# Kernel optimization log

Measured on AMD Instinct MI355X. Metric: run time of the kernel, lower is better.

## Reference

```python
import jax, jax.numpy as jnp
import numpy as np
from jax import lax

K = 8          # num_classes
C_IN = 256     # in_channels
EPS = 1e-5


def resize_bilinear_ac(x, H, W):
    """Bilinear resize with align_corners=True. x: [B,C,h,w] -> [B,C,H,W]."""
    B, C, h, w = x.shape
    if h == H and w == W:
        return x
    ys = jnp.linspace(0.0, h - 1.0, H)
    xs = jnp.linspace(0.0, w - 1.0, W)
    y0 = jnp.floor(ys).astype(jnp.int32)
    x0 = jnp.floor(xs).astype(jnp.int32)
    y1 = jnp.minimum(y0 + 1, h - 1)
    x1 = jnp.minimum(x0 + 1, w - 1)
    wy = (ys - y0.astype(x.dtype))[None, None, :, None]
    wx = (xs - x0.astype(x.dtype))[None, None, None, :]
    g00 = x[:, :, y0][:, :, :, x0]
    g01 = x[:, :, y0][:, :, :, x1]
    g10 = x[:, :, y1][:, :, :, x0]
    g11 = x[:, :, y1][:, :, :, x1]
    top = g00 * (1.0 - wx) + g01 * wx
    bot = g10 * (1.0 - wx) + g11 * wx
    return top * (1.0 - wy) + bot * wy


def setup_inputs() -> dict:
    key = jax.random.key(0)
    ks = jax.random.split(key, 16)
    shapes = [(2, 256, 128, 128), (2, 256, 64, 64), (2, 256, 32, 32), (2, 256, 16, 16), (2, 256, 8, 8)]
    inp = {}
    for i, s in enumerate(shapes):
        inp[f"feat{i}"] = jax.random.normal(ks[i], s, dtype=jnp.float32)
    inp["attr_feat"] = jax.random.normal(ks[5], (2, K * C_IN, 64, 64), dtype=jnp.float32)
    # learned params
    inp["mlp_f_w"] = jax.random.normal(ks[6], (256, 256), dtype=jnp.float32) * 0.02
    inp["mlp_f_b"] = jnp.zeros((256,), dtype=jnp.float32)
    inp["mlp_a_w"] = jax.random.normal(ks[7], (256, 256), dtype=jnp.float32) * 0.02
    inp["mlp_a_b"] = jnp.zeros((256,), dtype=jnp.float32)
    # 5 grouped convs: [out=2048, in_per_group=256, 3, 3] each, no bias (BN follows)
    inp["conv_w"] = jax.random.normal(ks[8], (5, K * C_IN, C_IN, 3, 3), dtype=jnp.float32) * 0.02
    inp["bn_gamma"] = jnp.ones((5, K * C_IN), dtype=jnp.float32)
    inp["bn_beta"] = jnp.zeros((5, K * C_IN), dtype=jnp.float32)
    inp["bn_mean"] = jax.random.normal(ks[9], (5, K * C_IN), dtype=jnp.float32) * 0.1
    inp["bn_var"] = jax.random.uniform(ks[10], (5, K * C_IN), dtype=jnp.float32, minval=0.5, maxval=1.5)
    return inp


def _forward(feats, attr_feat, mlp_f_w, mlp_f_b, mlp_a_w, mlp_a_b, conv_w, bn_gamma, bn_beta, bn_mean, bn_var):
    B = attr_feat.shape[0]
    # global avg pool attr -> [B, K, C] -> mlp_a
    avg_attr = attr_feat.mean(axis=(2, 3)).reshape(B, K, C_IN)
    avg_attr = avg_attr @ mlp_a_w.T + mlp_a_b  # [B,K,256]
    outs = []
    for i, x in enumerate(feats):
        _, C, H, W = x.shape
        avg_x = x.mean(axis=(2, 3)) @ mlp_f_w.T + mlp_f_b          # [B,256]
        logits = jnp.einsum('bkc,bc->bk', avg_attr, avg_x)          # [B,K]
        attn = jax.nn.softmax(logits, axis=-1)
        y = resize_bilinear_ac(attr_feat, H, W)                      # [B,2048,H,W]
        y = lax.conv_general_dilated(
            y, conv_w[i], window_strides=(1, 1), padding=((1, 1), (1, 1)),
            dimension_numbers=('NCHW', 'OIHW', 'NCHW'), feature_group_count=K)
        inv = lax.rsqrt(bn_var[i] + EPS)
        y = (y - bn_mean[i][None, :, None, None]) * (inv * bn_gamma[i])[None, :, None, None] + bn_beta[i][None, :, None, None]
        y = jax.nn.relu(y)
        y = y.reshape(B, K, C, H, W)
        y = jnp.einsum('bkchw,bk->bchw', y, attn)                   # weighted sum over classes
        outs.append(jax.nn.relu(x + y))
    return tuple(outs)


def reference(feat0, feat1, feat2, feat3, feat4, attr_feat, mlp_f_w, mlp_f_b, mlp_a_w, mlp_a_b, conv_w, bn_gamma, bn_beta, bn_mean, bn_var):
    feats = [feat0, feat1, feat2, feat3, feat4]
    return _forward(feats, attr_feat, mlp_f_w, mlp_f_b, mlp_a_w, mlp_a_b, conv_w, bn_gamma, bn_beta, bn_mean, bn_var)
```

## Files before the change

### kernel.cpp

```cpp
#include <hip/hip_runtime.h>
#include <hip/hip_bf16.h>
#include <cstdint>

typedef __attribute__((ext_vector_type(8))) short short8;
typedef __attribute__((ext_vector_type(4))) float f32x4;

#define EPSV 1e-5f

__device__ __forceinline__ void gload_lds16(const void* g, void* l) {
  __builtin_amdgcn_global_load_lds(
      (const __attribute__((address_space(1))) void*)(uintptr_t)g,
      (__attribute__((address_space(3))) void*)(uint32_t)(uintptr_t)l,
      16, 0, 0);
}

__device__ __forceinline__ uint32_t f2bf_rne(float v) {
  const uint32_t u = __float_as_uint(v);
  const uint32_t r = ((u >> 16) & 1u) + 0x7fffu;
  return (u + r) >> 16;
}

__global__ void mean_kernel(const float* __restrict__ in, float* __restrict__ out,
                            int HW, float inv) {
  const int ch = blockIdx.x;
  const int t = threadIdx.x;
  const float* p = in + (size_t)ch * HW;
  float s = 0.f;
  const int nv = HW >> 2;
  const float4* pv = (const float4*)p;
  for (int i = t; i < nv; i += 256) { float4 v = pv[i]; s += v.x + v.y + v.z + v.w; }
  __shared__ float red[256];
  red[t] = s; __syncthreads();
  for (int off = 128; off > 0; off >>= 1) {
    if (t < off) red[t] += red[t + off];
    __syncthreads();
  }
  if (t == 0) out[ch] = red[0] * inv;
}

__global__ void wtrans_kernel(const float* __restrict__ cw,
                              const float* __restrict__ gamma, const float* __restrict__ beta,
                              const float* __restrict__ mean, const float* __restrict__ var,
                              __hip_bfloat16* __restrict__ wt, float* __restrict__ bias) {
  const int oc = blockIdx.x;
  const int i  = blockIdx.y;
  const int ci = threadIdx.x;
  const int idx = i * 2048 + oc;
  const float sc = rsqrtf(var[idx] + EPSV) * gamma[idx];
  if (ci == 0) bias[idx] = beta[idx] - mean[idx] * sc;
  const int g = oc >> 8, co = oc & 255;
  const float* src = cw + ((size_t)idx * 256 + ci) * 9;
  const size_t dbase = (size_t)(i * 8 + g) * 9 * 65536 + co * 256 + ci;
#pragma unroll
  for (int tap = 0; tap < 9; ++tap)
    wt[dbase + (size_t)tap * 65536] = __float2bfloat16(src[tap] * sc);
}

__global__ void gate_kernel(const float* __restrict__ meanA, const float* __restrict__ meanF,
                            const float* __restrict__ Wa, const float* __restrict__ ba,
                            const float* __restrict__ Wf, const float* __restrict__ bfp,
                            float* __restrict__ attn) {
  __shared__ float mA[16 * 256];
  __shared__ float mF[10 * 256];
  __shared__ float pA[16 * 256];
  __shared__ float pF[10 * 256];
  __shared__ float lg[80];
  const int t = threadIdx.x;
  for (int i = t; i < 4096; i += 256) mA[i] = meanA[i];
  for (int i = t; i < 2560; i += 256) mF[i] = meanF[i];
  __syncthreads();
  {
    float acc[16];
#pragma unroll
    for (int j = 0; j < 16; ++j) acc[j] = 0.f;
    for (int ci = 0; ci < 256; ++ci) {
      const float w = Wa[t * 256 + ci];
#pragma unroll
      for (int j = 0; j < 16; ++j) acc[j] += mA[j * 256 + ci] * w;
    }
    const float bb = ba[t];
#pragma unroll
    for (int j = 0; j < 16; ++j) pA[j * 256 + t] = acc[j] + bb;
  }
  {
    float acc[10];
#pragma unroll
    for (int j = 0; j < 10; ++j) acc[j] = 0.f;
    for (int ci = 0; ci < 256; ++ci) {
      const float w = Wf[t * 256 + ci];
#pragma unroll
      for (int j = 0; j < 10; ++j) acc[j] += mF[j * 256 + ci] * w;
    }
    const float bb = bfp[t];
#pragma unroll
    for (int j = 0; j < 10; ++j) pF[j * 256 + t] = acc[j] + bb;
  }
  __syncthreads();
  if (t < 80) {
    const int i = t >> 4, r = t & 15, b = r >> 3, k = r & 7;
    const float* a = &pA[(b * 8 + k) * 256];
    const float* f = &pF[(i * 2 + b) * 256];
    float d = 0.f;
    for (int c = 0; c < 256; ++c) d += a[c] * f[c];
    lg[t] = d;
  }
  __syncthreads();
  if (t < 10) {
    const int base = t * 8;
    float m = lg[base];
    for (int k = 1; k < 8; ++k) m = fmaxf(m, lg[base + k]);
    float e[8], s = 0.f;
    for (int k = 0; k < 8; ++k) { e[k] = __expf(lg[base + k] - m); s += e[k]; }
    const float invs = 1.f / s;
    for (int k = 0; k < 8; ++k) attn[base + k] = e[k] * invs;
  }
}

__global__ void resize_kernel(const float* __restrict__ attr,
                              __hip_bfloat16* __restrict__ R,
                              int W, int Hp, int Wp, float scl) {
  const int bk = blockIdx.x;
  const int yp = blockIdx.y;
  const int t  = threadIdx.x;
  const size_t rowbase = ((size_t)bk * Hp + yp) * (size_t)Wp * 256;
  if (yp == 0 || yp == Hp - 1) {
    uint32_t* p = (uint32_t*)(R + rowbase);
    const int n = Wp * 128;
    for (int idx = t; idx < n; idx += 256) p[idx] = 0u;
    return;
  }
  const int y = yp - 1;
  const float fy = y * scl;
  int y0 = (int)floorf(fy); if (y0 > 63) y0 = 63;
  const float wy = fy - (float)y0;
  const int y1 = min(y0 + 1, 63);
  __shared__ float buf[2][64][65];
  const int cc = t >> 2, seg = (t & 3) * 16;
  const int bb = bk >> 3, k = bk & 7;
  const float* ab = attr + (size_t)bb * 2048 * 4096;
  const int ci = t & 63;
  for (int cq = 0; cq < 4; ++cq) {
    __syncthreads();
    {
      const int ch = k * 256 + cq * 64 + cc;
      const float* r0 = ab + ((size_t)ch * 64 + y0) * 64;
      const float* r1 = ab + ((size_t)ch * 64 + y1) * 64;
#pragma unroll
      for (int u = 0; u < 4; ++u) {
        float4 v0 = ((const float4*)r0)[(t & 3) * 4 + u];
        float4 v1 = ((const float4*)r1)[(t & 3) * 4 + u];
        buf[0][cc][seg + u * 4 + 0] = v0.x; buf[0][cc][seg + u * 4 + 1] = v0.y;
        buf[0][cc][seg + u * 4 + 2] = v0.z; buf[0][cc][seg + u * 4 + 3] = v0.w;
        buf[1][cc][seg + u * 4 + 0] = v1.x; buf[1][cc][seg + u * 4 + 1] = v1.y;
        buf[1][cc][seg + u * 4 + 2] = v1.z; buf[1][cc][seg + u * 4 + 3] = v1.w;
      }
    }
    __syncthreads();
    for (int x = t >> 6; x < W; x += 4) {
      const float fx = x * scl;
      int x0 = (int)floorf(fx); if (x0 > 63) x0 = 63;
      const float wx = fx - (float)x0;
      const int x1 = min(x0 + 1, 63);
      const float top = buf[0][ci][x0] * (1.f - wx) + buf[0][ci][x1] * wx;
      const float bot = buf[1][ci][x0] * (1.f - wx) + buf[1][ci][x1] * wx;
      R[rowbase + (size_t)(x + 1) * 256 + cq * 64 + ci] = __float2bfloat16(top * (1.f - wy) + bot * wy);
    }
    if (t < 64) {
      R[rowbase + cq * 64 + t] = __float2bfloat16(0.f);
      R[rowbase + (size_t)(Wp - 1) * 256 + cq * 64 + t] = __float2bfloat16(0.f);
    }
  }
}

__device__ __forceinline__ void coords36(int u, int g0, int& g, int& ty, int& tx, int& cq) {
  g = g0 + u / 36;
  const int r = u % 36;
  const int tap = r >> 2;
  cq = r & 3;
  ty = tap / 3;
  tx = tap - ty * 3;
}

__global__ __launch_bounds__(512, 1)
void conv256_kernel(const __hip_bfloat16* __restrict__ R,
                    const __hip_bfloat16* __restrict__ Wt,
                    const float* __restrict__ bias,
                    const float* __restrict__ attn,
                    __hip_bfloat16* __restrict__ zout,
                    int W, int lw, int Hp, int Wp, int HW,
                    int NB, int gcount) {
  __shared__ alignas(16) __hip_bfloat16 ldsA[2][256 * 64];
  __shared__ alignas(16) __hip_bfloat16 ldsB[2][256 * 64];
  const int tid  = threadIdx.x;
  const int lane = tid & 63;
  const int wave = __builtin_amdgcn_readfirstlane(tid >> 6);
  const int wm = (wave >> 2) * 128;
  const int wn = (wave & 3) * 64;

  const int nx  = gridDim.x;
  const int lin = blockIdx.x;
  const int pos = ((nx & 7) == 0) ? ((lin & 7) * (nx >> 3) + (lin >> 3)) : lin;
  const int n0  = pos * 256;

  const int bb = (int)blockIdx.y % NB;
  const int gs = (int)blockIdx.y / NB;
  const int g0 = gs * gcount;

  const int c8 = lane & 7, r8 = lane >> 3;
  const int sc = (c8 ^ r8) << 3;
  const int aoff0 = ((wave * 32 + r8) << 8) + sc;
  const int dst0  = wave * 2048;
  int boff[4];
#pragma unroll
  for (int q = 0; q < 4; ++q) {
    const int row = wave * 32 + q * 8 + r8;
    const int sg = n0 + row;
    const int y = sg >> lw, x = sg & (W - 1);
    boff[q] = ((y * Wp + x) << 8) + sc;
  }

  const size_t rgstride = (size_t)Hp * Wp * 256;
  const __hip_bfloat16* Rb = R + (size_t)bb * 8 * rgstride;

  const f32x4 fz = {0.f, 0.f, 0.f, 0.f};
  f32x4 acc[8][4];
  uint32_t finp[8][4][2];
#pragma unroll
  for (int mf = 0; mf < 8; ++mf)
#pragma unroll
    for (int nf = 0; nf < 4; ++nf) {
      acc[mf][nf] = fz; finp[mf][nf][0] = 0u; finp[mf][nf][1] = 0u;
    }

  const int nk = gcount * 36;
  {
    const __hip_bfloat16* wp = Wt + ((size_t)g0 * 9 << 16);
    const __hip_bfloat16* rp = Rb + (size_t)g0 * rgstride;
#pragma unroll
    for (int q = 0; q < 4; ++q) gload_lds16(wp + aoff0 + q * 2048, &ldsA[0][dst0 + q * 512]);
#pragma unroll
    for (int q = 0; q < 4; ++q) gload_lds16(rp + boff[q], &ldsB[0][dst0 + q * 512]);
  }

  int foldc = 0, gcur = g0;
  for (int t = 0; t < nk; ++t) {
    const int c = t & 1;
    const bool pf = (t + 1 < nk);
    int g1, ty1, tx1, cq1;
    coords36(pf ? t + 1 : t, g0, g1, ty1, tx1, cq1);
    const __hip_bfloat16* wp1 = Wt + (((size_t)g1 * 9 + ty1 * 3 + tx1) << 16) + (cq1 << 6);
    const __hip_bfloat16* rp1 = Rb + (size_t)g1 * rgstride + ((ty1 * Wp + tx1) << 8) + (cq1 << 6);

    asm volatile("s_waitcnt vmcnt(0)" ::: "memory");
    __builtin_amdgcn_s_barrier();
    asm volatile("" ::: "memory");

    const __hip_bfloat16* pA = &ldsA[c][0];
    const __hip_bfloat16* pB = &ldsB[c][0];
    __hip_bfloat16* dA = &ldsA[c ^ 1][0];
    __hip_bfloat16* dB = &ldsB[c ^ 1][0];

#pragma unroll
    for (int ks = 0; ks < 2; ++ks) {
      const int cb = ks * 4 + (lane >> 4);
      short8 bfv[4];
#pragma unroll
      for (int nf = 0; nf < 4; ++nf) {
        const int row = wn + nf * 16 + (lane & 15);
        bfv[nf] = *(const short8*)&pB[(row << 6) + ((cb ^ (row & 7)) << 3)];
      }
#pragma unroll
      for (int h = 0; h < 2; ++h) {
        short8 af[4];
#pragma unroll
        for (int m = 0; m < 4; ++m) {
          const int row = wm + (h * 4 + m) * 16 + (lane & 15);
          af[m] = *(const short8*)&pA[(row << 6) + ((cb ^ (row & 7)) << 3)];
        }
        if (ks == 0 && pf) {
          if (h == 0) {
#pragma unroll
            for (int q = 0; q < 4; ++q) gload_lds16(wp1 + aoff0 + q * 2048, dA + dst0 + q * 512);
          } else {
#pragma unroll
            for (int q = 0; q < 4; ++q) gload_lds16(rp1 + boff[q], dB + dst0 + q * 512);
          }
        }
        __builtin_amdgcn_s_barrier();
        __builtin_amdgcn_sched_barrier(0);
        __builtin_amdgcn_s_setprio(1);
#pragma unroll
        for (int m = 0; m < 4; ++m)
#pragma unroll
          for (int nf = 0; nf < 4; ++nf)
            acc[h * 4 + m][nf] = __builtin_amdgcn_mfma_f32_16x16x32_bf16(
                af[m], bfv[nf], acc[h * 4 + m][nf], 0, 0, 0);
        __builtin_amdgcn_s_setprio(0);
        __builtin_amdgcn_s_barrier();
        asm volatile("" ::: "memory");
      }
    }

    if (++foldc == 36) {
      foldc = 0;
      const float aw = attn[bb * 8 + gcur];
#pragma unroll
      for (int mf = 0; mf < 8; ++mf) {
        const int cobase = wm + mf * 16 + ((lane >> 4) << 2);
#pragma unroll
        for (int pr = 0; pr < 2; ++pr) {
          const float b0v = bias[(gcur << 8) + cobase + pr * 2 + 0];
          const float b1v = bias[(gcur << 8) + cobase + pr * 2 + 1];
#pragma unroll
          for (int nf = 0; nf < 4; ++nf) {
            const uint32_t p = finp[mf][nf][pr];
            const float f0 = __uint_as_float(p << 16)
                           + aw * fmaxf(acc[mf][nf][pr * 2 + 0] + b0v, 0.f);
            const float f1 = __uint_as_float(p & 0xffff0000u)
                           + aw * fmaxf(acc[mf][nf][pr * 2 + 1] + b1v, 0.f);
            finp[mf][nf][pr] = (f2bf_rne(f1) << 16) | f2bf_rne(f0);
          }
        }
#pragma unroll
        for (int nf = 0; nf < 4; ++nf) acc[mf][nf] = fz;
      }
      ++gcur;
    }
  }

  __hip_bfloat16* zb = zout + (size_t)(gs * 2 + bb) * 256 * (size_t)HW;
#pragma unroll
  for (int mf = 0; mf < 8; ++mf) {
    const int cobase = wm + mf * 16 + ((lane >> 4) << 2);
#pragma unroll
    for (int nf = 0; nf < 4; ++nf) {
      const int n = n0 + wn + nf * 16 + (lane & 15);
#pragma unroll
      for (int pr = 0; pr < 2; ++pr) {
        const uint32_t p = finp[mf][nf][pr];
        zb[(size_t)(cobase + pr * 2 + 0) * HW + n] =
            __float2bfloat16(__uint_as_float(p << 16));
        zb[(size_t)(cobase + pr * 2 + 1) * HW + n] =
            __float2bfloat16(__uint_as_float(p & 0xffff0000u));
      }
    }
  }
}

__global__ __launch_bounds__(256, 2)
void conv_kernel(const __hip_bfloat16* __restrict__ R,
                 const __hip_bfloat16* __restrict__ Wt,
                 const float* __restrict__ bias,
                 const float* __restrict__ attn,
                 const float* __restrict__ featp,
                 void* __restrict__ outp,
                 int W, int lw, int Hp, int Wp, int HW,
                 int b0, int NB, int gcount) {
  __shared__ alignas(16) __hip_bfloat16 ldsA[2][128 * 64];
  __shared__ alignas(16) __hip_bfloat16 ldsB[3][128 * 64];
  const int tid  = threadIdx.x;
  const int lane = tid & 63;
  const int wave = __builtin_amdgcn_readfirstlane(tid >> 6);
  const int wm = (wave >> 1) * 64;
  const int wn = (wave & 1) * 64;

  const int nx  = gridDim.x;
  const int lin = blockIdx.x;
  const int pos = ((nx & 7) == 0) ? ((lin & 7) * (nx >> 3) + (lin >> 3)) : lin;
  const int co0 = (pos & 1) * 128;
  const int n0  = (pos >> 1) * 128;

  const int bb  = (int)blockIdx.y % NB;
  const int gs  = (int)blockIdx.y / NB;
  const int b   = b0 + bb;
  const int g0  = gs * gcount;

  const int c8 = lane & 7;
  const int r8 = lane >> 3;
  int aoff[4], boff[4], dst[4];
#pragma unroll
  for (int q = 0; q < 4; ++q) {
    const int row = (wave * 4 + q) * 8 + r8;
    const int sc = (c8 ^ (row & 7)) << 3;
    aoff[q] = ((co0 + row) << 8) + sc;
    int sg = n0 + row; if (sg >= HW) sg = HW - 1;
    const int y = sg >> lw, x = sg & (W - 1);
    boff[q] = ((y * Wp + x) << 8) + sc;
    dst[q] = (wave * 4 + q) * 512;
  }

  const size_t rgstride = (size_t)Hp * Wp * 256;
  const __hip_bfloat16* Rb = R + (size_t)bb * 8 * rgstride;

  const f32x4 fz = {0.f, 0.f, 0.f, 0.f};
  f32x4 fin[4][4], acc[4][4];
#pragma unroll
  for (int mf = 0; mf < 4; ++mf)
#pragma unroll
    for (int nf = 0; nf < 4; ++nf) { fin[mf][nf] = fz; acc[mf][nf] = fz; }

  const int nstages = gcount * 36;
  {
    int g, ty, tx, cq;
    coords36(0, g0, g, ty, tx, cq);
    const __hip_bfloat16* wp = Wt + (((size_t)g * 9 + ty * 3 + tx) << 16) + (cq << 6);
    const __hip_bfloat16* rp = Rb + (size_t)g * rgstride + ((ty * Wp + tx) << 8) + (cq << 6);
#pragma unroll
    for (int q = 0; q < 4; ++q) gload_lds16(wp + aoff[q], &ldsA[0][dst[q]]);
#pragma unroll
    for (int q = 0; q < 4; ++q) gload_lds16(rp + boff[q], &ldsB[0][dst[q]]);
    coords36(1 < nstages ? 1 : 0, g0, g, ty, tx, cq);
    const __hip_bfloat16* rp1 = Rb + (size_t)g * rgstride + ((ty * Wp + tx) << 8) + (cq << 6);
#pragma unroll
    for (int q = 0; q < 4; ++q) gload_lds16(rp1 + boff[q], &ldsB[1][dst[q]]);
  }

  int bcur = 0, b2 = 2;
  int foldc = 0, gcur = g0;

  for (int s = 0; s < nstages; ++s) {
    __builtin_amdgcn_s_barrier();
    asm volatile("" ::: "memory");
    if (s + 1 < nstages) {
      int g, ty, tx, cq;
      coords36(s + 1, g0, g, ty, tx, cq);
      const __hip_bfloat16* wp = Wt + (((size_t)g * 9 + ty * 3 + tx) << 16) + (cq << 6);
      __hip_bfloat16* dA = &ldsA[(s + 1) & 1][0];
#pragma unroll
      for (int q = 0; q < 4; ++q) gload_lds16(wp + aoff[q], dA + dst[q]);
    }
    if (s + 2 < nstages) {
      int g, ty, tx, cq;
      coords36(s + 2, g0, g, ty, tx, cq);
      const __hip_bfloat16* rp = Rb + (size_t)g * rgstride + ((ty * Wp + tx) << 8) + (cq << 6);
      __hip_bfloat16* dB = &ldsB[b2][0];
#pragma unroll
      for (int q = 0; q < 4; ++q) gload_lds16(rp + boff[q], dB + dst[q]);
    }
    if (s + 2 < nstages)      asm volatile("s_waitcnt vmcnt(12)" ::: "memory");
    else if (s + 1 < nstages) asm volatile("s_waitcnt vmcnt(8)" ::: "memory");
    else                      asm volatile("s_waitcnt vmcnt(0)" ::: "memory");
    __builtin_amdgcn_s_barrier();
    asm volatile("" ::: "memory");

    const __hip_bfloat16* pA = &ldsA[s & 1][0];
    const __hip_bfloat16* pB = &ldsB[bcur][0];
#pragma unroll
    for (int ks = 0; ks < 2; ++ks) {
      short8 af[4], bfv[4];
      const int cb = ks * 4 + (lane >> 4);
#pragma unroll
      for (int mf = 0; mf < 4; ++mf) {
        const int row = wm + mf * 16 + (lane & 15);
        af[mf] = *(const short8*)&pA[(row << 6) + ((cb ^ (row & 7)) << 3)];
      }
#pragma unroll
      for (int nf = 0; nf < 4; ++nf) {
        const int row = wn + nf * 16 + (lane & 15);
        bfv[nf] = *(const short8*)&pB[(row << 6) + ((cb ^ (row & 7)) << 3)];
      }
#pragma unroll
      for (int mf = 0; mf < 4; ++mf)
#pragma unroll
        for (int nf = 0; nf < 4; ++nf)
          acc[mf][nf] = __builtin_amdgcn_mfma_f32_16x16x32_bf16(
              af[mf], bfv[nf], acc[mf][nf], 0, 0, 0);
    }

    if (++bcur == 3) bcur = 0;
    if (++b2 == 3) b2 = 0;

    if (++foldc == 36) {
      foldc = 0;
      const float aw = attn[b * 8 + gcur];
#pragma unroll
      for (int mf = 0; mf < 4; ++mf) {
        const int cobase = co0 + wm + mf * 16 + ((lane >> 4) << 2);
#pragma unroll
        for (int r = 0; r < 4; ++r) {
          const float bs = bias[(gcur << 8) + cobase + r];
#pragma unroll
          for (int nf = 0; nf < 4; ++nf) {
            fin[mf][nf][r] += aw * fmaxf(acc[mf][nf][r] + bs, 0.f);
            acc[mf][nf][r] = 0.f;
          }
        }
      }
      ++gcur;
    }
  }

  const size_t plane = (size_t)256 * HW;
  if (featp) {
    const float* fb = featp + (size_t)b * plane;
    float* ob = (float*)outp + (size_t)b * plane;
#pragma unroll
    for (int mf = 0; mf < 4; ++mf) {
      const int cobase = co0 + wm + mf * 16 + ((lane >> 4) << 2);
#pragma unroll
      for (int nf = 0; nf < 4; ++nf) {
        const int n = n0 + wn + nf * 16 + (lane & 15);
        if (n < HW) {
#pragma unroll
          for (int r = 0; r < 4; ++r) {
            const size_t idx = (size_t)(cobase + r) * HW + n;
            ob[idx] = fmaxf(fb[idx] + fin[mf][nf][r], 0.f);
          }
        }
      }
    }
  } else {
    __hip_bfloat16* zb = (__hip_bfloat16*)outp + ((size_t)gs * 2 + b) * plane;
#pragma unroll
    for (int mf = 0; mf < 4; ++mf) {
      const int cobase = co0 + wm + mf * 16 + ((lane >> 4) << 2);
#pragma unroll
      for (int nf = 0; nf < 4; ++nf) {
        const int n = n0 + wn + nf * 16 + (lane & 15);
        if (n < HW) {
#pragma unroll
          for (int r = 0; r < 4; ++r)
            zb[(size_t)(cobase + r) * HW + n] = __float2bfloat16(fin[mf][nf][r]);
        }
      }
    }
  }
}

__global__ void reduce_kernel(const __hip_bfloat16* __restrict__ z,
                              const float* __restrict__ feat,
                              float* __restrict__ outp, int total, int S) {
  const int i4 = (blockIdx.x * 256 + threadIdx.x) * 4;
  if (i4 >= total) return;
  float4 f = *(const float4*)(feat + i4);
  float s0 = f.x, s1 = f.y, s2 = f.z, s3 = f.w;
  for (int j = 0; j < S; ++j) {
    const ushort4 v = *(const ushort4*)(z + (size_t)j * total + i4);
    s0 += __uint_as_float((uint32_t)v.x << 16);
    s1 += __uint_as_float((uint32_t)v.y << 16);
    s2 += __uint_as_float((uint32_t)v.z << 16);
    s3 += __uint_as_float((uint32_t)v.w << 16);
  }
  float4 o = {fmaxf(s0, 0.f), fmaxf(s1, 0.f), fmaxf(s2, 0.f), fmaxf(s3, 0.f)};
  *(float4*)(outp + i4) = o;
}

extern "C" void kernel_launch(void* const* d_in, const int* in_sizes, int n_in,
                              void* d_out, int out_size, void* d_ws, size_t ws_size,
                              hipStream_t stream) {
  const float* feat[5];
  for (int i = 0; i < 5; ++i) feat[i] = (const float*)d_in[i];
  const float* attr = (const float*)d_in[5];
  const float* mfw = (const float*)d_in[6];
  const float* mfb = (const float*)d_in[7];
  const float* maw = (const float*)d_in[8];
  const float* mab = (const float*)d_in[9];
  const float* cw  = (const float*)d_in[10];
  const float* bng = (const float*)d_in[11];
  const float* bnb = (const float*)d_in[12];
  const float* bnm = (const float*)d_in[13];
  const float* bnv = (const float*)d_in[14];
  float* out = (float*)d_out;

  char* ws = (char*)d_ws;
  float* attnW = (float*)(ws);
  float* meanA = (float*)(ws + 512);
  float* meanF = (float*)(ws + 20480);
  float* biasW = (float*)(ws + 32768);
  __hip_bfloat16* Wt = (__hip_bfloat16*)(ws + 131072);
  const size_t R_OFF = 47316992;
  __hip_bfloat16* Rbuf = (__hip_bfloat16*)(ws + R_OFF);

  const bool full = ws_size >= (size_t)219316224;
  const int NB = full ? 2 : 1;
  __hip_bfloat16* zbuf = (__hip_bfloat16*)(ws + R_OFF + (size_t)NB * 69222400);

  static const int HS[5] = {128, 64, 32, 16, 8};
  static const size_t OOFF[5] = {0, 8388608, 10485760, 11010048, 11141120};

  mean_kernel<<<4096, 256, 0, stream>>>(attr, meanA, 4096, 1.f / 4096.f);
  for (int i = 0; i < 5; ++i) {
    const int HW = HS[i] * HS[i];
    mean_kernel<<<512, 256, 0, stream>>>(feat[i], meanF + i * 512, HW, 1.f / (float)HW);
  }
  wtrans_kernel<<<dim3(2048, 5), 256, 0, stream>>>(cw, bng, bnb, bnm, bnv, Wt, biasW);
  gate_kernel<<<1, 256, 0, stream>>>(meanA, meanF, maw, mab, mfw, mfb, attnW);

  for (int i = 0; i < 5; ++i) {
    const int H = HS[i], W = H, HW = H * W, Hp = H + 2, Wp = W + 2;
    const int lw = 31 - __builtin_clz((unsigned)W);
    const float scl = 63.f / (float)(H - 1);

    if (full) {
      resize_kernel<<<dim3(16, Hp), 256, 0, stream>>>(attr, Rbuf, W, Hp, Wp, scl);
      if (i <= 1) {
        const int S = (i == 0) ? 2 : 8;
        const int gcount = 8 / S;
        conv256_kernel<<<dim3(HW / 256, 2 * S), 512, 0, stream>>>(
            Rbuf, Wt + (size_t)i * 8 * 9 * 65536, biasW + i * 2048, attnW + i * 16,
            zbuf, W, lw, Hp, Wp, HW, 2, gcount);
        const int total = 2 * 256 * HW;
        reduce_kernel<<<(total / 4 + 255) / 256, 256, 0, stream>>>(
            zbuf, feat[i], out + OOFF[i], total, S);
      } else {
        const int ntiles = (HW + 127) / 128;
        conv_kernel<<<dim3(ntiles * 2, 2 * 8), 256, 0, stream>>>(
            Rbuf, Wt + (size_t)i * 8 * 9 * 65536, biasW + i * 2048, attnW + i * 16,
            nullptr, zbuf, W, lw, Hp, Wp, HW, 0, 2, 1);
        const int total = 2 * 256 * HW;
        reduce_kernel<<<(total / 4 + 255) / 256, 256, 0, stream>>>(
            zbuf, feat[i], out + OOFF[i], total, 8);
      }
    } else {
      const int ntiles = (HW + 127) / 128;
      for (int b0 = 0; b0 < 2; ++b0) {
        resize_kernel<<<dim3(8, Hp), 256, 0, stream>>>(
            attr + (size_t)b0 * 2048 * 4096, Rbuf, W, Hp, Wp, scl);
        conv_kernel<<<dim3(ntiles * 2, 1), 256, 0, stream>>>(
            Rbuf, Wt + (size_t)i * 8 * 9 * 65536, biasW + i * 2048, attnW + i * 16,
            feat[i], out + OOFF[i], W, lw, Hp, Wp, HW, b0, 1, 8);
      }
    }
  }
}
```

Measured before the change: 723.9 us.

## Fuse feature mean launches, stage conv weights in LDS, remap conv block order

Five per-scale mean launches become one kernel that picks the scale from the block index. The weight-transform kernel now loads each output channel's contiguous 2304-float slice into shared memory with coalesced reads, instead of strided 9-float reads per thread. The conv kernel uses a new 2D block-index swizzle when the grid holds exactly 256 blocks, spreading work across XCDs. These aim to cut launch overhead, uncoalesced global loads and cache locality problems, at the cost of more shared memory in wtrans and a grid-size-specific mapping.

```diff
diff --git a/kernel.cpp b/kernel.cpp
--- a/kernel.cpp
+++ b/kernel.cpp
@@ -18,6 +18,9 @@
   const uint32_t u = __float_as_uint(v);
   const uint32_t r = ((u >> 16) & 1u) + 0x7fffu;
   return (u + r) >> 16;
+}
+__device__ __forceinline__ float bf2f(uint32_t u) {
+  return __uint_as_float(u << 16);
 }
 
 __global__ void mean_kernel(const float* __restrict__ in, float* __restrict__ out,
@@ -38,22 +41,54 @@
   if (t == 0) out[ch] = red[0] * inv;
 }
 
+__global__ void meanf_kernel(const float* __restrict__ f0, const float* __restrict__ f1,
+                             const float* __restrict__ f2, const float* __restrict__ f3,
+                             const float* __restrict__ f4, float* __restrict__ out) {
+  const int scale = blockIdx.x >> 9;
+  const int ch = blockIdx.x & 511;
+  const int t = threadIdx.x;
+  const float* base;
+  int HW;
+  switch (scale) {
+    case 0: base = f0; HW = 16384; break;
+    case 1: base = f1; HW = 4096;  break;
+    case 2: base = f2; HW = 1024;  break;
+    case 3: base = f3; HW = 256;   break;
+    default: base = f4; HW = 64;   break;
+  }
+  const float* p = base + (size_t)ch * HW;
+  float s = 0.f;
+  const int nv = HW >> 2;
+  const float4* pv = (const float4*)p;
+  for (int i = t; i < nv; i += 256) { float4 v = pv[i]; s += v.x + v.y + v.z + v.w; }
+  __shared__ float red[256];
+  red[t] = s; __syncthreads();
+  for (int off = 128; off > 0; off >>= 1) {
+    if (t < off) red[t] += red[t + off];
+    __syncthreads();
+  }
+  if (t == 0) out[scale * 512 + ch] = red[0] / (float)HW;
+}
+
 __global__ void wtrans_kernel(const float* __restrict__ cw,
                               const float* __restrict__ gamma, const float* __restrict__ beta,
                               const float* __restrict__ mean, const float* __restrict__ var,
                               __hip_bfloat16* __restrict__ wt, float* __restrict__ bias) {
+  __shared__ float wl[2304];
   const int oc = blockIdx.x;
   const int i  = blockIdx.y;
-  const int ci = threadIdx.x;
+  const int t  = threadIdx.x;
   const int idx = i * 2048 + oc;
+  const float* src = cw + (size_t)idx * 2304;
+  for (int e = t; e < 2304; e += 256) wl[e] = src[e];
+  __syncthreads();
   const float sc = rsqrtf(var[idx] + EPSV) * gamma[idx];
-  if (ci == 0) bias[idx] = beta[idx] - mean[idx] * sc;
+  if (t == 0) bias[idx] = beta[idx] - mean[idx] * sc;
   const int g = oc >> 8, co = oc & 255;
-  const float* src = cw + ((size_t)idx * 256 + ci) * 9;
-  const size_t dbase = (size_t)(i * 8 + g) * 9 * 65536 + co * 256 + ci;
+  const size_t dbase = (size_t)(i * 8 + g) * 9 * 65536 + co * 256 + t;
 #pragma unroll
   for (int tap = 0; tap < 9; ++tap)
-    wt[dbase + (size_t)tap * 65536] = __float2bfloat16(src[tap] * sc);
+    wt[dbase + (size_t)tap * 65536] = __float2bfloat16(wl[t * 9 + tap] * sc);
 }
 
 __global__ void gate_kernel(const float* __restrict__ meanA, const float* __restrict__ meanF,
@@ -197,13 +232,16 @@
   const int wm = (wave >> 2) * 128;
   const int wn = (wave & 3) * 64;
 
-  const int nx  = gridDim.x;
-  const int lin = blockIdx.x;
-  const int pos = ((nx & 7) == 0) ? ((lin & 7) * (nx >> 3) + (lin >> 3)) : lin;
-  const int n0  = pos * 256;
-
-  const int bb = (int)blockIdx.y % NB;
-  const int gs = (int)blockIdx.y / NB;
+  const int X = gridDim.x;
+  int xp = blockIdx.x, yv = blockIdx.y;
+  if (X * gridDim.y == 256) {
+    const int lin2 = blockIdx.x + X * blockIdx.y;
+    const int d = (lin2 & 7) * 32 + (lin2 >> 3);
+    yv = d / X; xp = d - yv * X;
+  }
+  const int n0 = xp * 256;
+  const int bb = yv % NB;
+  const int gs = yv / NB;
   const int g0 = gs * gcount;
 
   const int c8 = lane & 7, r8 = lane >> 3;
@@ -536,10 +574,10 @@
   float s0 = f.x, s1 = f.y, s2 = f.z, s3 = f.w;
   for (int j = 0; j < S; ++j) {
     const ushort4 v = *(const ushort4*)(z + (size_t)j * total + i4);
-    s0 += __uint_as_float((uint32_t)v.x << 16);
-    s1 += __uint_as_float((uint32_t)v.y << 16);
-    s2 += __uint_as_float((uint32_t)v.z << 16);
-    s3 += __uint_as_float((uint32_t)v.w << 16);
+    s0 += bf2f(v.x);
+    s1 += bf2f(v.y);
+    s2 += bf2f(v.z);
+    s3 += bf2f(v.w);
   }
   float4 o = {fmaxf(s0, 0.f), fmaxf(s1, 0.f), fmaxf(s2, 0.f), fmaxf(s3, 0.f)};
   *(float4*)(outp + i4) = o;
@@ -579,10 +617,7 @@
   static const size_t OOFF[5] = {0, 8388608, 10485760, 11010048, 11141120};
 
   mean_kernel<<<4096, 256, 0, stream>>>(attr, meanA, 4096, 1.f / 4096.f);
-  for (int i = 0; i < 5; ++i) {
-    const int HW = HS[i] * HS[i];
-    mean_kernel<<<512, 256, 0, stream>>>(feat[i], meanF + i * 512, HW, 1.f / (float)HW);
-  }
+  meanf_kernel<<<2560, 256, 0, stream>>>(feat[0], feat[1], feat[2], feat[3], feat[4], meanF);
   wtrans_kernel<<<dim3(2048, 5), 256, 0, stream>>>(cw, bng, bnb, bnm, bnv, Wt, biasW);
   gate_kernel<<<1, 256, 0, stream>>>(meanA, meanF, maw, mab, mfw, mfb, attnW);
 
```

Measured after the change: 724.8 us. About the same (+0.1%).
